# Kernel optimization log

Hardware: AMD Instinct MI355X
Metric: run time of the kernel (lower is better)

## Reference

```python
import jax, jax.numpy as jnp
import numpy as np

N = 100000      # nodes
D = 128         # per-component feature dim
E = 3200000     # edges (avg degree 32)
NUM_CLS = 40
EPS = 1e-7


def lorentz_logmap0(x):
    # Lorentz model, curvature -1, origin o = (1, 0, ..., 0).
    # log_o(x) = arccosh(x0) * (x - x0*o) / ||x - x0*o||  ; keeps full dim, time comp -> 0
    x0 = x[..., :1]
    u = jnp.concatenate([jnp.zeros_like(x0), x[..., 1:]], axis=-1)
    un = jnp.sqrt(jnp.clip(x0 * x0 - 1.0, EPS))
    return jnp.arccosh(jnp.maximum(x0, 1.0)) * u / un


def sphere_logmap0(x):
    # Unit sphere, origin o = (1, 0, ..., 0).
    # log_o(x) = arccos(<o,x>) * (x - <o,x> o) / ||x - <o,x> o||
    c = x[..., :1]
    u = jnp.concatenate([jnp.zeros_like(c), x[..., 1:]], axis=-1)
    un = jnp.sqrt(jnp.clip(1.0 - c * c, EPS))
    return jnp.arccos(jnp.clip(c, -1.0, 1.0)) * u / un


def setup_inputs() -> dict:
    key = jax.random.key(0)
    k1, k2, k3, k4, k5 = jax.random.split(key, 5)
    x_E = jax.random.normal(k1, (N, D), jnp.float32)
    # valid hyperboloid points: x0 = sqrt(1 + ||rest||^2)
    rest = 0.5 * jax.random.normal(k2, (N, D - 1), jnp.float32)
    x0 = jnp.sqrt(1.0 + jnp.sum(rest * rest, axis=-1, keepdims=True))
    x_H = jnp.concatenate([x0, rest], axis=-1)
    # valid sphere points: unit norm
    xs = jax.random.normal(k3, (N, D), jnp.float32)
    x_S = xs / jnp.linalg.norm(xs, axis=-1, keepdims=True)
    W = jax.random.normal(k4, (3 * D, NUM_CLS), jnp.float32) / np.sqrt(3 * D)
    edge_index = jax.random.randint(k5, (2, E), 0, N, dtype=jnp.int32)
    return {"x_E": x_E, "x_H": x_H, "x_S": x_S, "W": W, "edge_index": edge_index}


def reference(x_E, x_H, x_S, W, edge_index):
    # logmap0 projections + concat
    x = jnp.concatenate([x_E, lorentz_logmap0(x_H), sphere_logmap0(x_S)], axis=-1)  # [N, 3D]
    # GCNConv(bias=False): transform first (num_cls << in_dim), then normalized aggregation
    h = x @ W  # [N, C]
    row, col = edge_index[0], edge_index[1]
    loop = jnp.arange(N, dtype=edge_index.dtype)
    row = jnp.concatenate([row, loop])
    col = jnp.concatenate([col, loop])
    deg = jax.ops.segment_sum(jnp.ones_like(col, dtype=h.dtype), col, num_segments=N)
    dinv = jnp.where(deg > 0, jax.lax.rsqrt(jnp.maximum(deg, 1.0)), 0.0)
    norm = dinv[row] * dinv[col]  # [E+N]
    out = jax.ops.segment_sum(h[row] * norm[:, None], col, num_segments=N)  # [N, C]
    return out
```

## Files before the change

### kernel.cpp

```cpp
#include <hip/hip_runtime.h>
#include <math.h>

constexpr int NN   = 100000;
constexpr int DIM  = 128;
constexpr int NE   = 3200000;
constexpr int NCLS = 40;
constexpr float EPSF = 1e-7f;

constexpr int BSH  = 9;
constexpr int BSZ  = 1 << BSH;
constexpr int NBKT = (NN + BSZ - 1) >> BSH;
constexpr int CAP  = 18432;
constexpr int AEPB = 4096;
constexpr int ABLK = (NE + AEPB - 1) / AEPB;

constexpr int GSTR = 64;

typedef __attribute__((ext_vector_type(8))) short bf16x8;
typedef __attribute__((ext_vector_type(8))) unsigned short u16x8;
typedef __attribute__((ext_vector_type(4))) float f32x4;

__device__ __forceinline__ unsigned short f2bf(float f) {
    unsigned u = __builtin_bit_cast(unsigned, f);
    unsigned r = u + 0x7FFFu + ((u >> 16) & 1u);
    return (unsigned short)(r >> 16);
}
__device__ __forceinline__ float bf2f(unsigned short b) {
    return __builtin_bit_cast(float, (unsigned)b << 16);
}

__global__ __launch_bounds__(256) void binA_kernel(const int* __restrict__ row,
                                                   const int* __restrict__ col,
                                                   int* __restrict__ gcur,
                                                   unsigned* __restrict__ pairs) {
    __shared__ int hist[256];
    __shared__ int lofx[256];
    __shared__ int gbase[256];
    __shared__ unsigned sortedw[AEPB];
    __shared__ int dstg[AEPB];

    int t = threadIdx.x;
    int e0 = blockIdx.x * AEPB;
    int cnt = min(AEPB, NE - e0);

    hist[t] = 0;
    __syncthreads();
    for (int k = t; k < cnt; k += 256) atomicAdd(&hist[col[e0 + k] >> BSH], 1);
    __syncthreads();

    int h = hist[t];
    if (t < NBKT && h > 0) gbase[t] = atomicAdd(&gcur[t], h);
    lofx[t] = h;
    __syncthreads();
    for (int d = 1; d < 256; d <<= 1) {
        int o = (t >= d) ? lofx[t - d] : 0;
        __syncthreads();
        lofx[t] += o;
        __syncthreads();
    }
    int excl = lofx[t] - h;
    lofx[t] = excl;
    hist[t] = excl;
    __syncthreads();

    for (int k = t; k < cnt; k += 256) {
        int c = col[e0 + k], r = row[e0 + k];
        int b = c >> BSH;
        int pos = atomicAdd(&hist[b], 1);
        sortedw[pos] = ((unsigned)(c & (BSZ - 1)) << 17) | (unsigned)r;
        dstg[pos] = b * CAP + gbase[b] + (pos - lofx[b]);
    }
    __syncthreads();
    for (int k = t; k < cnt; k += 256) pairs[dstg[k]] = sortedw[k];
}

__global__ __launch_bounds__(256) void bscan_kernel(const int* __restrict__ gcur,
                                                    int* __restrict__ bbase) {
    __shared__ int sc[256];
    int t = threadIdx.x;
    int v = (t < NBKT) ? gcur[t] : 0;
    sc[t] = v;
    __syncthreads();
    for (int d = 1; d < 256; d <<= 1) {
        int o = (t >= d) ? sc[t - d] : 0;
        __syncthreads();
        sc[t] += o;
        __syncthreads();
    }
    if (t < NBKT) bbase[t] = sc[t] - v;
}

__global__ __launch_bounds__(1024) void binB_kernel(const int* __restrict__ gcur,
                                                    const int* __restrict__ bbase,
                                                    const unsigned* __restrict__ pairs,
                                                    int* __restrict__ ebuf,
                                                    int* __restrict__ offs) {
    __shared__ unsigned in[CAP];
    __shared__ int srow[CAP];
    __shared__ int hist[512];
    __shared__ int sc[1024];

    int t = threadIdx.x;
    int b = blockIdx.x;
    int cnt = gcur[b];
    int base = bbase[b];
    const unsigned* pb = pairs + (size_t)b * CAP;

    for (int i = t; i < cnt; i += 1024) in[i] = pb[i];
    if (t < 512) hist[t] = 0;
    __syncthreads();
    for (int i = t; i < cnt; i += 1024) atomicAdd(&hist[in[i] >> 17], 1);
    __syncthreads();

    int v = (t < 512) ? hist[t] : 0;
    sc[t] = v;
    __syncthreads();
    for (int d = 1; d < 1024; d <<= 1) {
        int o = (t >= d) ? sc[t - d] : 0;
        __syncthreads();
        sc[t] += o;
        __syncthreads();
    }
    int excl = sc[t] - v;
    if (t < 512) {
        int c = (b << BSH) + t;
        if (c <= NN) offs[c] = base + excl;
        hist[t] = excl;
    }
    __syncthreads();
    for (int i = t; i < cnt; i += 1024) {
        unsigned w = in[i];
        int pos = atomicAdd(&hist[w >> 17], 1);
        srow[pos] = (int)(w & 0x1FFFFu);
    }
    __syncthreads();
    for (int i = t; i < cnt; i += 1024) ebuf[base + i] = srow[i];
}

__global__ __launch_bounds__(256) void wpack_kernel(const float* __restrict__ W,
                                                    unsigned short* __restrict__ wbf) {
    int idx = blockIdx.x * 256 + threadIdx.x;
    if (idx >= 12 * 3 * 2 * 64 * 8) return;
    int j    = idx & 7;
    int lane = (idx >> 3) & 63;
    int hl   = (idx >> 9) & 1;
    int rest = idx >> 10;
    int t    = rest % 3;
    int kc   = rest / 3;
    int k = kc * 32 + 8 * (lane >> 4) + j;
    int c = 16 * t + (lane & 15);
    float w = (c < NCLS) ? W[k * NCLS + c] : 0.f;
    unsigned short hi = f2bf(w);
    wbf[idx] = (hl == 0) ? hi : f2bf(w - bf2f(hi));
}

__global__ __launch_bounds__(256) void h_kernel(
    const float* __restrict__ xE, const float* __restrict__ xH,
    const float* __restrict__ xS, const unsigned short* __restrict__ wbf,
    const int* __restrict__ offs, unsigned short* __restrict__ gbf) {

    int t = threadIdx.x;
    int lane = t & 63;
    int wv = t >> 6;
    int n0 = blockIdx.x * 64;
    int r  = lane & 15;
    int kq = lane >> 4;
    int myrow = n0 + 16 * wv + r;
    bool rowok = myrow < NN;

    f32x4 acc0 = {0.f, 0.f, 0.f, 0.f};
    f32x4 acc1 = acc0, acc2 = acc0;

    const bf16x8* wfr = reinterpret_cast<const bf16x8*>(wbf);

    for (int m = 0; m < 3; ++m) {
        const float* xb = (m == 0) ? xE : (m == 1) ? xH : xS;
        const float* xrow = xb + (size_t)myrow * DIM;

        float4 xf[8];
#pragma unroll
        for (int kc4 = 0; kc4 < 4; ++kc4) {
            int off = kc4 * 32 + kq * 8;
            xf[2 * kc4]     = rowok ? *reinterpret_cast<const float4*>(xrow + off)
                                    : make_float4(0.f, 0.f, 0.f, 0.f);
            xf[2 * kc4 + 1] = rowok ? *reinterpret_cast<const float4*>(xrow + off + 4)
                                    : make_float4(0.f, 0.f, 0.f, 0.f);
        }

        float scm = 1.f;
        if (m > 0) {
            float x0 = rowok ? xrow[0] : 1.f;
            if (m == 1) {
                scm = acoshf(fmaxf(x0, 1.f)) * rsqrtf(fmaxf(x0 * x0 - 1.f, EPSF));
            } else {
                float cc = fminf(fmaxf(x0, -1.f), 1.f);
                scm = acosf(cc) * rsqrtf(fmaxf(1.f - x0 * x0, EPSF));
            }
        }

#pragma unroll
        for (int kc4 = 0; kc4 < 4; ++kc4) {
            float4 f0 = xf[2 * kc4], f1 = xf[2 * kc4 + 1];
            float a[8] = {f0.x, f0.y, f0.z, f0.w, f1.x, f1.y, f1.z, f1.w};
            if (m > 0 && kc4 == 0 && kq == 0) a[0] = 0.f;

            bf16x8 ah, al;
#pragma unroll
            for (int j = 0; j < 8; ++j) {
                float av = a[j] * scm;
                unsigned short hbits = f2bf(av);
                ah[j] = (short)hbits;
                al[j] = (short)f2bf(av - bf2f(hbits));
            }

            int kc = m * 4 + kc4;
            const bf16x8* wb = wfr + (size_t)(kc * 3) * 2 * 64;
            bf16x8 bh0 = wb[0 * 128 + 0 * 64 + lane];
            bf16x8 bl0 = wb[0 * 128 + 1 * 64 + lane];
            bf16x8 bh1 = wb[1 * 128 + 0 * 64 + lane];
            bf16x8 bl1 = wb[1 * 128 + 1 * 64 + lane];
            bf16x8 bh2 = wb[2 * 128 + 0 * 64 + lane];
            bf16x8 bl2 = wb[2 * 128 + 1 * 64 + lane];

            acc0 = __builtin_amdgcn_mfma_f32_16x16x32_bf16(ah, bh0, acc0, 0, 0, 0);
            acc0 = __builtin_amdgcn_mfma_f32_16x16x32_bf16(al, bh0, acc0, 0, 0, 0);
            acc0 = __builtin_amdgcn_mfma_f32_16x16x32_bf16(ah, bl0, acc0, 0, 0, 0);
            acc1 = __builtin_amdgcn_mfma_f32_16x16x32_bf16(ah, bh1, acc1, 0, 0, 0);
            acc1 = __builtin_amdgcn_mfma_f32_16x16x32_bf16(al, bh1, acc1, 0, 0, 0);
            acc1 = __builtin_amdgcn_mfma_f32_16x16x32_bf16(ah, bl1, acc1, 0, 0, 0);
            acc2 = __builtin_amdgcn_mfma_f32_16x16x32_bf16(ah, bh2, acc2, 0, 0, 0);
            acc2 = __builtin_amdgcn_mfma_f32_16x16x32_bf16(al, bh2, acc2, 0, 0, 0);
            acc2 = __builtin_amdgcn_mfma_f32_16x16x32_bf16(ah, bl2, acc2, 0, 0, 0);
        }
    }

    int nbase = n0 + 16 * wv + 4 * kq;
    int4 oa = make_int4(0, 0, 0, 0);
    int ob = 0;
    if (nbase < NN) {
        oa = *reinterpret_cast<const int4*>(offs + nbase);
        ob = offs[min(nbase + 4, NN)];
    }
    int dg[4] = {oa.y - oa.x, oa.z - oa.y, oa.w - oa.z, ob - oa.w};

#pragma unroll
    for (int i = 0; i < 4; ++i) {
        int n = nbase + i;
        if (n < NN) {
            float di = rsqrtf((float)(dg[i] + 1));
            unsigned short* gr = gbf + (size_t)n * GSTR;
            gr[r]      = f2bf(acc0[i] * di);
            gr[16 + r] = f2bf(acc1[i] * di);
            if (r < 8)
                gr[32 + r] = f2bf(acc2[i] * di);
        }
    }
}

__global__ __launch_bounds__(256) void gather_kernel(
    const int* __restrict__ offs, const int* __restrict__ ebuf,
    const unsigned short* __restrict__ gbf, float* __restrict__ out) {
    int t = blockIdx.x * blockDim.x + threadIdx.x;
    if (t >= NN * 5) return;
    int n  = t / 5;
    int c8 = t - n * 5;

    const u16x8* gb = reinterpret_cast<const u16x8*>(gbf) + c8;
    int s = offs[n], e = offs[n + 1];
    float dinv = rsqrtf((float)(e - s + 1));

    u16x8 sv = gb[n * 8];
    float a0[8], a1[8], a2[8], a3[8];
#pragma unroll
    for (int k = 0; k < 8; ++k) {
        a0[k] = bf2f(sv[k]); a1[k] = 0.f; a2[k] = 0.f; a3[k] = 0.f;
    }

    int j = s;
    for (; j + 3 < e; j += 4) {
        int r0 = ebuf[j], r1 = ebuf[j + 1], r2 = ebuf[j + 2], r3 = ebuf[j + 3];
        u16x8 v0 = gb[r0 * 8];
        u16x8 v1 = gb[r1 * 8];
        u16x8 v2 = gb[r2 * 8];
        u16x8 v3 = gb[r3 * 8];
#pragma unroll
        for (int k = 0; k < 8; ++k) {
            a0[k] += bf2f(v0[k]); a1[k] += bf2f(v1[k]);
            a2[k] += bf2f(v2[k]); a3[k] += bf2f(v3[k]);
        }
    }
    for (; j < e; ++j) {
        u16x8 v = gb[ebuf[j] * 8];
#pragma unroll
        for (int k = 0; k < 8; ++k) a0[k] += bf2f(v[k]);
    }

    float* on = out + (size_t)n * NCLS + c8 * 8;
    float4 o0, o1;
    o0.x = (a0[0] + a1[0] + a2[0] + a3[0]) * dinv;
    o0.y = (a0[1] + a1[1] + a2[1] + a3[1]) * dinv;
    o0.z = (a0[2] + a1[2] + a2[2] + a3[2]) * dinv;
    o0.w = (a0[3] + a1[3] + a2[3] + a3[3]) * dinv;
    o1.x = (a0[4] + a1[4] + a2[4] + a3[4]) * dinv;
    o1.y = (a0[5] + a1[5] + a2[5] + a3[5]) * dinv;
    o1.z = (a0[6] + a1[6] + a2[6] + a3[6]) * dinv;
    o1.w = (a0[7] + a1[7] + a2[7] + a3[7]) * dinv;
    *reinterpret_cast<float4*>(on)     = o0;
    *reinterpret_cast<float4*>(on + 4) = o1;
}

extern "C" void kernel_launch(void* const* d_in, const int* in_sizes, int n_in,
                              void* d_out, int out_size, void* d_ws, size_t ws_size,
                              hipStream_t stream) {
    const float* xE = (const float*)d_in[0];
    const float* xH = (const float*)d_in[1];
    const float* xS = (const float*)d_in[2];
    const float* W  = (const float*)d_in[3];
    const int*   ei = (const int*)d_in[4];
    const int* row = ei;
    const int* col = ei + NE;
    float* out = (float*)d_out;

    auto pad = [](size_t x) { return (x + 255) & ~(size_t)255; };
    char* p = (char*)d_ws;
    int* gcur  = (int*)p;               p += pad((size_t)NBKT * 4);
    int* bbase = (int*)p;               p += pad((size_t)NBKT * 4);
    int* offs  = (int*)p;               p += pad((size_t)(NN + 1) * 4);
    int* ebuf  = (int*)p;               p += pad((size_t)NE * 4);
    unsigned* pairs = (unsigned*)p;
    unsigned short* gbf = (unsigned short*)p;
    p += pad((size_t)NBKT * CAP * 4);
    unsigned short* wbf = (unsigned short*)p;

    hipMemsetAsync(gcur, 0, (size_t)NBKT * 4, stream);

    wpack_kernel<<<(12 * 3 * 2 * 64 * 8 + 255) / 256, 256, 0, stream>>>(W, wbf);
    binA_kernel<<<ABLK, 256, 0, stream>>>(row, col, gcur, pairs);
    bscan_kernel<<<1, 256, 0, stream>>>(gcur, bbase);
    binB_kernel<<<NBKT, 1024, 0, stream>>>(gcur, bbase, pairs, ebuf, offs);
    h_kernel<<<(NN + 63) / 64, 256, 0, stream>>>(xE, xH, xS, wbf, offs, gbf);
    gather_kernel<<<(NN * 5 + 255) / 256, 256, 0, stream>>>(offs, ebuf, gbf, out);
}
```

Baseline: 157.7 us.

## Split h_kernel K-loop across three waves per row tile with LDS reduction

Each 64-node block now runs 12 waves instead of 4: one wave group per manifold component (E, H, S), each doing a third of the K dimension. The partial accumulators are written to shared memory and summed after a barrier, then scaled by the degree normalization and stored as bf16. This is meant to give more memory-level parallelism for the row loads in the h-transform. In exchange it adds a sizeable LDS buffer, a block-wide sync and scalar 2-byte output stores.

```diff
diff --git a/kernel.cpp b/kernel.cpp
--- a/kernel.cpp
+++ b/kernel.cpp
@@ -154,105 +154,112 @@
     wbf[idx] = (hl == 0) ? hi : f2bf(w - bf2f(hi));
 }
 
-__global__ __launch_bounds__(256) void h_kernel(
+__global__ __launch_bounds__(768) void h_kernel(
     const float* __restrict__ xE, const float* __restrict__ xH,
     const float* __restrict__ xS, const unsigned short* __restrict__ wbf,
     const int* __restrict__ offs, unsigned short* __restrict__ gbf) {
 
+    __shared__ float part[12 * 40 * 17];
+    __shared__ int loffs[65];
+
     int t = threadIdx.x;
     int lane = t & 63;
-    int wv = t >> 6;
+    int wave = t >> 6;
+    int m  = wave >> 2;
+    int wv = wave & 3;
     int n0 = blockIdx.x * 64;
     int r  = lane & 15;
     int kq = lane >> 4;
     int myrow = n0 + 16 * wv + r;
     bool rowok = myrow < NN;
 
+    if (t < 65) loffs[t] = offs[min(n0 + t, NN)];
+
     f32x4 acc0 = {0.f, 0.f, 0.f, 0.f};
     f32x4 acc1 = acc0, acc2 = acc0;
 
     const bf16x8* wfr = reinterpret_cast<const bf16x8*>(wbf);
-
-    for (int m = 0; m < 3; ++m) {
-        const float* xb = (m == 0) ? xE : (m == 1) ? xH : xS;
-        const float* xrow = xb + (size_t)myrow * DIM;
-
-        float4 xf[8];
-#pragma unroll
-        for (int kc4 = 0; kc4 < 4; ++kc4) {
-            int off = kc4 * 32 + kq * 8;
-            xf[2 * kc4]     = rowok ? *reinterpret_cast<const float4*>(xrow + off)
-                                    : make_float4(0.f, 0.f, 0.f, 0.f);
-            xf[2 * kc4 + 1] = rowok ? *reinterpret_cast<const float4*>(xrow + off + 4)
-                                    : make_float4(0.f, 0.f, 0.f, 0.f);
+    const float* xb = (m == 0) ? xE : (m == 1) ? xH : xS;
+    const float* xrow = xb + (size_t)myrow * DIM;
+
+    float4 xf[8];
+#pragma unroll
+    for (int kc4 = 0; kc4 < 4; ++kc4) {
+        int off = kc4 * 32 + kq * 8;
+        xf[2 * kc4]     = rowok ? *reinterpret_cast<const float4*>(xrow + off)
+                                : make_float4(0.f, 0.f, 0.f, 0.f);
+        xf[2 * kc4 + 1] = rowok ? *reinterpret_cast<const float4*>(xrow + off + 4)
+                                : make_float4(0.f, 0.f, 0.f, 0.f);
+    }
+
+    float scm = 1.f;
+    if (m > 0) {
+        float x0 = rowok ? xrow[0] : 1.f;
+        if (m == 1) {
+            scm = acoshf(fmaxf(x0, 1.f)) * rsqrtf(fmaxf(x0 * x0 - 1.f, EPSF));
+        } else {
+            float cc = fminf(fmaxf(x0, -1.f), 1.f);
+            scm = acosf(cc) * rsqrtf(fmaxf(1.f - x0 * x0, EPSF));
         }
-
-        float scm = 1.f;
-        if (m > 0) {
-            float x0 = rowok ? xrow[0] : 1.f;
-            if (m == 1) {
-                scm = acoshf(fmaxf(x0, 1.f)) * rsqrtf(fmaxf(x0 * x0 - 1.f, EPSF));
-            } else {
-                float cc = fminf(fmaxf(x0, -1.f), 1.f);
-                scm = acosf(cc) * rsqrtf(fmaxf(1.f - x0 * x0, EPSF));
-            }
+    }
+
+#pragma unroll
+    for (int kc4 = 0; kc4 < 4; ++kc4) {
+        float4 f0 = xf[2 * kc4], f1 = xf[2 * kc4 + 1];
+        float a[8] = {f0.x, f0.y, f0.z, f0.w, f1.x, f1.y, f1.z, f1.w};
+        if (m > 0 && kc4 == 0 && kq == 0) a[0] = 0.f;
+
+        bf16x8 ah, al;
+#pragma unroll
+        for (int j = 0; j < 8; ++j) {
+            float av = a[j] * scm;
+            unsigned short hbits = f2bf(av);
+            ah[j] = (short)hbits;
+            al[j] = (short)f2bf(av - bf2f(hbits));
         }
 
-#pragma unroll
-        for (int kc4 = 0; kc4 < 4; ++kc4) {
-            float4 f0 = xf[2 * kc4], f1 = xf[2 * kc4 + 1];
-            float a[8] = {f0.x, f0.y, f0.z, f0.w, f1.x, f1.y, f1.z, f1.w};
-            if (m > 0 && kc4 == 0 && kq == 0) a[0] = 0.f;
-
-            bf16x8 ah, al;
-#pragma unroll
-            for (int j = 0; j < 8; ++j) {
-                float av = a[j] * scm;
-                unsigned short hbits = f2bf(av);
-                ah[j] = (short)hbits;
-                al[j] = (short)f2bf(av - bf2f(hbits));
-            }
-
-            int kc = m * 4 + kc4;
-            const bf16x8* wb = wfr + (size_t)(kc * 3) * 2 * 64;
-            bf16x8 bh0 = wb[0 * 128 + 0 * 64 + lane];
-            bf16x8 bl0 = wb[0 * 128 + 1 * 64 + lane];
-            bf16x8 bh1 = wb[1 * 128 + 0 * 64 + lane];
-            bf16x8 bl1 = wb[1 * 128 + 1 * 64 + lane];
-            bf16x8 bh2 = wb[2 * 128 + 0 * 64 + lane];
-            bf16x8 bl2 = wb[2 * 128 + 1 * 64 + lane];
-
-            acc0 = __builtin_amdgcn_mfma_f32_16x16x32_bf16(ah, bh0, acc0, 0, 0, 0);
-            acc0 = __builtin_amdgcn_mfma_f32_16x16x32_bf16(al, bh0, acc0, 0, 0, 0);
-            acc0 = __builtin_amdgcn_mfma_f32_16x16x32_bf16(ah, bl0, acc0, 0, 0, 0);
-            acc1 = __builtin_amdgcn_mfma_f32_16x16x32_bf16(ah, bh1, acc1, 0, 0, 0);
-            acc1 = __builtin_amdgcn_mfma_f32_16x16x32_bf16(al, bh1, acc1, 0, 0, 0);
-            acc1 = __builtin_amdgcn_mfma_f32_16x16x32_bf16(ah, bl1, acc1, 0, 0, 0);
-            acc2 = __builtin_amdgcn_mfma_f32_16x16x32_bf16(ah, bh2, acc2, 0, 0, 0);
-            acc2 = __builtin_amdgcn_mfma_f32_16x16x32_bf16(al, bh2, acc2, 0, 0, 0);
-            acc2 = __builtin_amdgcn_mfma_f32_16x16x32_bf16(ah, bl2, acc2, 0, 0, 0);
-        }
-    }
-
-    int nbase = n0 + 16 * wv + 4 * kq;
-    int4 oa = make_int4(0, 0, 0, 0);
-    int ob = 0;
-    if (nbase < NN) {
-        oa = *reinterpret_cast<const int4*>(offs + nbase);
-        ob = offs[min(nbase + 4, NN)];
-    }
-    int dg[4] = {oa.y - oa.x, oa.z - oa.y, oa.w - oa.z, ob - oa.w};
+        int kc = m * 4 + kc4;
+        const bf16x8* wb = wfr + (size_t)(kc * 3) * 2 * 64;
+        bf16x8 bh0 = wb[0 * 128 + 0 * 64 + lane];
+        bf16x8 bl0 = wb[0 * 128 + 1 * 64 + lane];
+        bf16x8 bh1 = wb[1 * 128 + 0 * 64 + lane];
+        bf16x8 bl1 = wb[1 * 128 + 1 * 64 + lane];
+        bf16x8 bh2 = wb[2 * 128 + 0 * 64 + lane];
+        bf16x8 bl2 = wb[2 * 128 + 1 * 64 + lane];
+
+        acc0 = __builtin_amdgcn_mfma_f32_16x16x32_bf16(ah, bh0, acc0, 0, 0, 0);
+        acc0 = __builtin_amdgcn_mfma_f32_16x16x32_bf16(al, bh0, acc0, 0, 0, 0);
+        acc0 = __builtin_amdgcn_mfma_f32_16x16x32_bf16(ah, bl0, acc0, 0, 0, 0);
+        acc1 = __builtin_amdgcn_mfma_f32_16x16x32_bf16(ah, bh1, acc1, 0, 0, 0);
+        acc1 = __builtin_amdgcn_mfma_f32_16x16x32_bf16(al, bh1, acc1, 0, 0, 0);
+        acc1 = __builtin_amdgcn_mfma_f32_16x16x32_bf16(ah, bl1, acc1, 0, 0, 0);
+        acc2 = __builtin_amdgcn_mfma_f32_16x16x32_bf16(ah, bh2, acc2, 0, 0, 0);
+        acc2 = __builtin_amdgcn_mfma_f32_16x16x32_bf16(al, bh2, acc2, 0, 0, 0);
+        acc2 = __builtin_amdgcn_mfma_f32_16x16x32_bf16(ah, bl2, acc2, 0, 0, 0);
+    }
 
 #pragma unroll
     for (int i = 0; i < 4; ++i) {
-        int n = nbase + i;
+        int node = 4 * kq + i;
+        part[(wave * 40 + r) * 17 + node]      = acc0[i];
+        part[(wave * 40 + 16 + r) * 17 + node] = acc1[i];
+        if (r < 8)
+            part[(wave * 40 + 32 + r) * 17 + node] = acc2[i];
+    }
+    __syncthreads();
+
+    for (int o = t; o < 64 * NCLS; o += 768) {
+        int node = o / NCLS;
+        int c = o - node * NCLS;
+        int wvn = node >> 4, nl = node & 15;
+        float s = part[((0 * 4 + wvn) * 40 + c) * 17 + nl]
+                + part[((1 * 4 + wvn) * 40 + c) * 17 + nl]
+                + part[((2 * 4 + wvn) * 40 + c) * 17 + nl];
+        int n = n0 + node;
         if (n < NN) {
-            float di = rsqrtf((float)(dg[i] + 1));
-            unsigned short* gr = gbf + (size_t)n * GSTR;
-            gr[r]      = f2bf(acc0[i] * di);
-            gr[16 + r] = f2bf(acc1[i] * di);
-            if (r < 8)
-                gr[32 + r] = f2bf(acc2[i] * di);
+            int deg = loffs[node + 1] - loffs[node];
+            float di = rsqrtf((float)(deg + 1));
+            gbf[(size_t)n * GSTR + c] = f2bf(s * di);
         }
     }
 }
@@ -338,6 +345,6 @@
     binA_kernel<<<ABLK, 256, 0, stream>>>(row, col, gcur, pairs);
     bscan_kernel<<<1, 256, 0, stream>>>(gcur, bbase);
     binB_kernel<<<NBKT, 1024, 0, stream>>>(gcur, bbase, pairs, ebuf, offs);
-    h_kernel<<<(NN + 63) / 64, 256, 0, stream>>>(xE, xH, xS, wbf, offs, gbf);
+    h_kernel<<<(NN + 63) / 64, 768, 0, stream>>>(xE, xH, xS, wbf, offs, gbf);
     gather_kernel<<<(NN * 5 + 255) / 256, 256, 0, stream>>>(offs, ebuf, gbf, out);
 }
```

New measurement: 159.3 us. About the same (+1.0%).

## Fuse bucket sort into gather kernel and compute degree via separate histogram pass

Applied to the files above, without the earlier changes.

Removes the global CSR build (bscan plus binB writing ebuf/offs). A light dinv_kernel histograms each bucket to get inverse-sqrt degrees for h_kernel. A fused kernel then re-sorts each bucket in shared memory and gathers neighbor features straight from the LDS row list. This drops the ebuf/offs global round trip and one launch. The cost is a second pass over the pairs buffer, and the gather now runs on only ~196 large blocks, which may reduce parallelism and latency hiding.

```diff
diff --git a/kernel.cpp b/kernel.cpp
--- a/kernel.cpp
+++ b/kernel.cpp
@@ -74,67 +74,22 @@
     for (int k = t; k < cnt; k += 256) pairs[dstg[k]] = sortedw[k];
 }
 
-__global__ __launch_bounds__(256) void bscan_kernel(const int* __restrict__ gcur,
-                                                    int* __restrict__ bbase) {
-    __shared__ int sc[256];
-    int t = threadIdx.x;
-    int v = (t < NBKT) ? gcur[t] : 0;
-    sc[t] = v;
-    __syncthreads();
-    for (int d = 1; d < 256; d <<= 1) {
-        int o = (t >= d) ? sc[t - d] : 0;
-        __syncthreads();
-        sc[t] += o;
-        __syncthreads();
-    }
-    if (t < NBKT) bbase[t] = sc[t] - v;
-}
-
-__global__ __launch_bounds__(1024) void binB_kernel(const int* __restrict__ gcur,
-                                                    const int* __restrict__ bbase,
+__global__ __launch_bounds__(1024) void dinv_kernel(const int* __restrict__ gcur,
                                                     const unsigned* __restrict__ pairs,
-                                                    int* __restrict__ ebuf,
-                                                    int* __restrict__ offs) {
-    __shared__ unsigned in[CAP];
-    __shared__ int srow[CAP];
-    __shared__ int hist[512];
-    __shared__ int sc[1024];
-
+                                                    float* __restrict__ dinvt) {
+    __shared__ int hist[BSZ];
     int t = threadIdx.x;
     int b = blockIdx.x;
+    if (t < BSZ) hist[t] = 0;
+    __syncthreads();
     int cnt = gcur[b];
-    int base = bbase[b];
     const unsigned* pb = pairs + (size_t)b * CAP;
-
-    for (int i = t; i < cnt; i += 1024) in[i] = pb[i];
-    if (t < 512) hist[t] = 0;
-    __syncthreads();
-    for (int i = t; i < cnt; i += 1024) atomicAdd(&hist[in[i] >> 17], 1);
-    __syncthreads();
-
-    int v = (t < 512) ? hist[t] : 0;
-    sc[t] = v;
-    __syncthreads();
-    for (int d = 1; d < 1024; d <<= 1) {
-        int o = (t >= d) ? sc[t - d] : 0;
-        __syncthreads();
-        sc[t] += o;
-        __syncthreads();
-    }
-    int excl = sc[t] - v;
-    if (t < 512) {
-        int c = (b << BSH) + t;
-        if (c <= NN) offs[c] = base + excl;
-        hist[t] = excl;
-    }
-    __syncthreads();
-    for (int i = t; i < cnt; i += 1024) {
-        unsigned w = in[i];
-        int pos = atomicAdd(&hist[w >> 17], 1);
-        srow[pos] = (int)(w & 0x1FFFFu);
-    }
-    __syncthreads();
-    for (int i = t; i < cnt; i += 1024) ebuf[base + i] = srow[i];
+    for (int i = t; i < cnt; i += 1024) atomicAdd(&hist[pb[i] >> 17], 1);
+    __syncthreads();
+    if (t < BSZ) {
+        int n = (b << BSH) + t;
+        if (n < NN) dinvt[n] = rsqrtf((float)(hist[t] + 1));
+    }
 }
 
 __global__ __launch_bounds__(256) void wpack_kernel(const float* __restrict__ W,
@@ -157,7 +112,7 @@
 __global__ __launch_bounds__(256) void h_kernel(
     const float* __restrict__ xE, const float* __restrict__ xH,
     const float* __restrict__ xS, const unsigned short* __restrict__ wbf,
-    const int* __restrict__ offs, unsigned short* __restrict__ gbf) {
+    const float* __restrict__ dinvt, unsigned short* __restrict__ gbf) {
 
     int t = threadIdx.x;
     int lane = t & 63;
@@ -235,19 +190,16 @@
     }
 
     int nbase = n0 + 16 * wv + 4 * kq;
-    int4 oa = make_int4(0, 0, 0, 0);
-    int ob = 0;
-    if (nbase < NN) {
-        oa = *reinterpret_cast<const int4*>(offs + nbase);
-        ob = offs[min(nbase + 4, NN)];
-    }
-    int dg[4] = {oa.y - oa.x, oa.z - oa.y, oa.w - oa.z, ob - oa.w};
+    float4 dv = make_float4(0.f, 0.f, 0.f, 0.f);
+    if (nbase < NN)
+        dv = *reinterpret_cast<const float4*>(dinvt + nbase);
+    float dg[4] = {dv.x, dv.y, dv.z, dv.w};
 
 #pragma unroll
     for (int i = 0; i < 4; ++i) {
         int n = nbase + i;
         if (n < NN) {
-            float di = rsqrtf((float)(dg[i] + 1));
+            float di = dg[i];
             unsigned short* gr = gbf + (size_t)n * GSTR;
             gr[r]      = f2bf(acc0[i] * di);
             gr[16 + r] = f2bf(acc1[i] * di);
@@ -257,56 +209,97 @@
     }
 }
 
-__global__ __launch_bounds__(256) void gather_kernel(
-    const int* __restrict__ offs, const int* __restrict__ ebuf,
+__global__ __launch_bounds__(1024) void fusedBG_kernel(
+    const int* __restrict__ gcur, const unsigned* __restrict__ pairs,
     const unsigned short* __restrict__ gbf, float* __restrict__ out) {
-    int t = blockIdx.x * blockDim.x + threadIdx.x;
-    if (t >= NN * 5) return;
-    int n  = t / 5;
-    int c8 = t - n * 5;
-
-    const u16x8* gb = reinterpret_cast<const u16x8*>(gbf) + c8;
-    int s = offs[n], e = offs[n + 1];
-    float dinv = rsqrtf((float)(e - s + 1));
-
-    u16x8 sv = gb[n * 8];
-    float a0[8], a1[8], a2[8], a3[8];
-#pragma unroll
-    for (int k = 0; k < 8; ++k) {
-        a0[k] = bf2f(sv[k]); a1[k] = 0.f; a2[k] = 0.f; a3[k] = 0.f;
-    }
-
-    int j = s;
-    for (; j + 3 < e; j += 4) {
-        int r0 = ebuf[j], r1 = ebuf[j + 1], r2 = ebuf[j + 2], r3 = ebuf[j + 3];
-        u16x8 v0 = gb[r0 * 8];
-        u16x8 v1 = gb[r1 * 8];
-        u16x8 v2 = gb[r2 * 8];
-        u16x8 v3 = gb[r3 * 8];
+
+    __shared__ unsigned in[CAP];
+    __shared__ int srow[CAP];
+    __shared__ int hist[512];
+    __shared__ int sc[1024];
+
+    int t = threadIdx.x;
+    int b = blockIdx.x;
+    int cnt = gcur[b];
+    const unsigned* pb = pairs + (size_t)b * CAP;
+
+    for (int i = t; i < cnt; i += 1024) in[i] = pb[i];
+    if (t < 512) hist[t] = 0;
+    __syncthreads();
+    for (int i = t; i < cnt; i += 1024) atomicAdd(&hist[in[i] >> 17], 1);
+    __syncthreads();
+
+    int v = (t < 512) ? hist[t] : 0;
+    sc[t] = v;
+    __syncthreads();
+    for (int d = 1; d < 1024; d <<= 1) {
+        int o = (t >= d) ? sc[t - d] : 0;
+        __syncthreads();
+        sc[t] += o;
+        __syncthreads();
+    }
+    int excl = sc[t] - v;
+    __syncthreads();
+    if (t < 512) { sc[t] = excl; hist[t] = excl; }
+    __syncthreads();
+
+    for (int i = t; i < cnt; i += 1024) {
+        unsigned w = in[i];
+        int pos = atomicAdd(&hist[w >> 17], 1);
+        srow[pos] = (int)(w & 0x1FFFFu);
+    }
+    __syncthreads();
+
+    const u16x8* gball = reinterpret_cast<const u16x8*>(gbf);
+    for (int task = t; task < BSZ * 5; task += 1024) {
+        int c  = task / 5;
+        int c8 = task - c * 5;
+        int n = (b << BSH) + c;
+        if (n >= NN) continue;
+        int s = sc[c];
+        int e = (c == BSZ - 1) ? cnt : sc[c + 1];
+        float dinv = rsqrtf((float)(e - s + 1));
+
+        const u16x8* gb = gball + c8;
+        u16x8 sv = gb[(size_t)n * 8];
+        float a0[8], a1[8], a2[8], a3[8];
 #pragma unroll
         for (int k = 0; k < 8; ++k) {
-            a0[k] += bf2f(v0[k]); a1[k] += bf2f(v1[k]);
-            a2[k] += bf2f(v2[k]); a3[k] += bf2f(v3[k]);
-        }
-    }
-    for (; j < e; ++j) {
-        u16x8 v = gb[ebuf[j] * 8];
-#pragma unroll
-        for (int k = 0; k < 8; ++k) a0[k] += bf2f(v[k]);
-    }
-
-    float* on = out + (size_t)n * NCLS + c8 * 8;
-    float4 o0, o1;
-    o0.x = (a0[0] + a1[0] + a2[0] + a3[0]) * dinv;
-    o0.y = (a0[1] + a1[1] + a2[1] + a3[1]) * dinv;
-    o0.z = (a0[2] + a1[2] + a2[2] + a3[2]) * dinv;
-    o0.w = (a0[3] + a1[3] + a2[3] + a3[3]) * dinv;
-    o1.x = (a0[4] + a1[4] + a2[4] + a3[4]) * dinv;
-    o1.y = (a0[5] + a1[5] + a2[5] + a3[5]) * dinv;
-    o1.z = (a0[6] + a1[6] + a2[6] + a3[6]) * dinv;
-    o1.w = (a0[7] + a1[7] + a2[7] + a3[7]) * dinv;
-    *reinterpret_cast<float4*>(on)     = o0;
-    *reinterpret_cast<float4*>(on + 4) = o1;
+            a0[k] = bf2f(sv[k]); a1[k] = 0.f; a2[k] = 0.f; a3[k] = 0.f;
+        }
+
+        int j = s;
+        for (; j + 3 < e; j += 4) {
+            int r0 = srow[j], r1 = srow[j + 1], r2 = srow[j + 2], r3 = srow[j + 3];
+            u16x8 v0 = gb[(size_t)r0 * 8];
+            u16x8 v1 = gb[(size_t)r1 * 8];
+            u16x8 v2 = gb[(size_t)r2 * 8];
+            u16x8 v3 = gb[(size_t)r3 * 8];
+#pragma unroll
+            for (int k = 0; k < 8; ++k) {
+                a0[k] += bf2f(v0[k]); a1[k] += bf2f(v1[k]);
+                a2[k] += bf2f(v2[k]); a3[k] += bf2f(v3[k]);
+            }
+        }
+        for (; j < e; ++j) {
+            u16x8 vv = gb[(size_t)srow[j] * 8];
+#pragma unroll
+            for (int k = 0; k < 8; ++k) a0[k] += bf2f(vv[k]);
+        }
+
+        float* on = out + (size_t)n * NCLS + c8 * 8;
+        float4 o0, o1;
+        o0.x = (a0[0] + a1[0] + a2[0] + a3[0]) * dinv;
+        o0.y = (a0[1] + a1[1] + a2[1] + a3[1]) * dinv;
+        o0.z = (a0[2] + a1[2] + a2[2] + a3[2]) * dinv;
+        o0.w = (a0[3] + a1[3] + a2[3] + a3[3]) * dinv;
+        o1.x = (a0[4] + a1[4] + a2[4] + a3[4]) * dinv;
+        o1.y = (a0[5] + a1[5] + a2[5] + a3[5]) * dinv;
+        o1.z = (a0[6] + a1[6] + a2[6] + a3[6]) * dinv;
+        o1.w = (a0[7] + a1[7] + a2[7] + a3[7]) * dinv;
+        *reinterpret_cast<float4*>(on)     = o0;
+        *reinterpret_cast<float4*>(on + 4) = o1;
+    }
 }
 
 extern "C" void kernel_launch(void* const* d_in, const int* in_sizes, int n_in,
@@ -323,21 +316,18 @@
 
     auto pad = [](size_t x) { return (x + 255) & ~(size_t)255; };
     char* p = (char*)d_ws;
-    int* gcur  = (int*)p;               p += pad((size_t)NBKT * 4);
-    int* bbase = (int*)p;               p += pad((size_t)NBKT * 4);
-    int* offs  = (int*)p;               p += pad((size_t)(NN + 1) * 4);
-    int* ebuf  = (int*)p;               p += pad((size_t)NE * 4);
-    unsigned* pairs = (unsigned*)p;
+    int* gcur = (int*)p;                p += pad((size_t)NBKT * 4);
+    unsigned* pairs = (unsigned*)p;     p += pad((size_t)NBKT * CAP * 4);
     unsigned short* gbf = (unsigned short*)p;
-    p += pad((size_t)NBKT * CAP * 4);
+    p += pad((size_t)NN * GSTR * 2);
+    float* dinvt = (float*)p;           p += pad((size_t)NN * 4);
     unsigned short* wbf = (unsigned short*)p;
 
     hipMemsetAsync(gcur, 0, (size_t)NBKT * 4, stream);
 
     wpack_kernel<<<(12 * 3 * 2 * 64 * 8 + 255) / 256, 256, 0, stream>>>(W, wbf);
     binA_kernel<<<ABLK, 256, 0, stream>>>(row, col, gcur, pairs);
-    bscan_kernel<<<1, 256, 0, stream>>>(gcur, bbase);
-    binB_kernel<<<NBKT, 1024, 0, stream>>>(gcur, bbase, pairs, ebuf, offs);
-    h_kernel<<<(NN + 63) / 64, 256, 0, stream>>>(xE, xH, xS, wbf, offs, gbf);
-    gather_kernel<<<(NN * 5 + 255) / 256, 256, 0, stream>>>(offs, ebuf, gbf, out);
-}
+    dinv_kernel<<<NBKT, 1024, 0, stream>>>(gcur, pairs, dinvt);
+    h_kernel<<<(NN + 63) / 64, 256, 0, stream>>>(xE, xH, xS, wbf, dinvt, gbf);
+    fusedBG_kernel<<<NBKT, 1024, 0, stream>>>(gcur, pairs, gbf, out);
+}
```

After: 144.3 us. 1.09x faster.
